# Performance work log

Measured on AMD Instinct MI355X. Metric: run time of the kernel, lower is better.

The kernel has to match this reference:

```python
import jax, jax.numpy as jnp
import numpy as np

INDEX_SHIFT = jnp.array([[0, 0], [-1, 0], [1, 0], [0, 1], [-1, 1], [1, 1], [0, -1], [-1, -1], [1, -1]], dtype=jnp.int32)
H, W = 320, 320
C = 32          # embed_dim / feat_channels (hard-coded 32 in module)
NH = 2          # head_num
HD = C // NH    # per-head dim
B, N = 4, 20000


def setup_inputs() -> dict:
    key = jax.random.key(0)
    ks = jax.random.split(key, 8)

    def coords(k):
        # unique (y, x) coords per sample so the coord->index lookup is well defined
        perm = jax.random.permutation(k, H * W)[:N]
        return jnp.stack([perm // W, perm % W], axis=-1).astype(jnp.int32)

    li_coors = jax.vmap(coords)(jax.random.split(ks[0], B))
    ra_coors = jax.vmap(coords)(jax.random.split(ks[1], B))
    li_feats = jax.random.normal(ks[2], (B, N, C), jnp.float32)
    ra_feats = jax.random.normal(ks[3], (B, N, C), jnp.float32)
    pos = jax.random.normal(ks[4], (9, C), jnp.float32) * 0.02

    s = 1.0 / np.sqrt(C)
    out = {"li_bev_feats": li_feats, "li_bev_coors": li_coors,
           "ra_bev_feats": ra_feats, "ra_bev_coors": ra_coors,
           "pos_embedding": pos}
    for i, kk in [(1, ks[5]), (2, ks[6])]:
        k0, k1 = jax.random.split(kk)
        out[f"in_w{i}"] = jax.random.uniform(k0, (3 * C, C), jnp.float32, -s, s)
        out[f"in_b{i}"] = jnp.zeros((3 * C,), jnp.float32)
        out[f"out_w{i}"] = jax.random.uniform(k1, (C, C), jnp.float32, -s, s)
        out[f"out_b{i}"] = jnp.zeros((C,), jnp.float32)
    return out


def _build_kv(q_coors, kv_coors, kv_feats, pos):
    # q_coors, kv_coors: (N,2) int; kv_feats: (N,C)
    n = q_coors.shape[0]
    grid = jnp.full((H * W,), -1, jnp.int32)
    grid = grid.at[kv_coors[:, 0] * W + kv_coors[:, 1]].set(jnp.arange(n, dtype=jnp.int32))
    sc = q_coors[None, :, :] + INDEX_SHIFT[:, None, :]            # (9,N,2)
    valid = (sc[..., 0] >= 0) & (sc[..., 0] < H) & (sc[..., 1] >= 0) & (sc[..., 1] < W)
    flat = jnp.clip(sc[..., 0], 0, H - 1) * W + jnp.clip(sc[..., 1], 0, W - 1)
    sel = jnp.where(valid, grid[flat], -1)                        # (9,N)
    mask = (sel >= 0)[..., None]                                  # (9,N,1)
    g = kv_feats[jnp.maximum(sel, 0)]                             # (9,N,C)
    k = jnp.where(mask, g, 0.0)
    v = jnp.where(mask, g + pos[:, None, :], 0.0)
    return k.transpose(1, 0, 2), v.transpose(1, 0, 2)             # (N,9,C)


def _mha(q, k, v, in_w, in_b, out_w, out_b):
    # q: (N,C); k,v: (N,L,C). torch MultiheadAttention (eval mode, dropout off).
    n, L = k.shape[0], k.shape[1]
    wq, wk, wv = in_w[:C], in_w[C:2 * C], in_w[2 * C:]
    bq, bk, bv = in_b[:C], in_b[C:2 * C], in_b[2 * C:]
    qh = (q @ wq.T + bq).reshape(n, NH, HD)
    kh = (k @ wk.T + bk).reshape(n, L, NH, HD)
    vh = (v @ wv.T + bv).reshape(n, L, NH, HD)
    scores = jnp.einsum('nhd,nlhd->nhl', qh, kh) / np.sqrt(HD)
    attn = jax.nn.softmax(scores, axis=-1)
    o = jnp.einsum('nhl,nlhd->nhd', attn, vh).reshape(n, C)
    return o @ out_w.T + out_b


def _scatter(feats, coors):
    # PointPillarsScatter: place (N,C) feats at (y,x) into a (C,H,W) canvas
    idx = coors[:, 0] * W + coors[:, 1]
    canvas = jnp.zeros((C, H * W), feats.dtype)
    return canvas.at[:, idx].set(feats.T).reshape(C, H, W)


def reference(li_bev_feats, li_bev_coors, ra_bev_feats, ra_bev_coors, pos_embedding,
              in_w1, in_b1, out_w1, out_b1, in_w2, in_b2, out_w2, out_b2):
    def one(li_f, li_c, ra_f, ra_c):
        k, v = _build_kv(li_c, ra_c, ra_f, pos_embedding)
        li_img = _scatter(_mha(li_f, k, v, in_w1, in_b1, out_w1, out_b1), li_c)
        k, v = _build_kv(ra_c, li_c, li_f, pos_embedding)
        ra_img = _scatter(_mha(ra_f, k, v, in_w2, in_b2, out_w2, out_b2), ra_c)
        return li_img, ra_img
    li_imgs, ra_imgs = jax.vmap(one)(li_bev_feats, li_bev_coors, ra_bev_feats, ra_bev_coors)
    return li_imgs, ra_imgs  # each (B, C, H, W)
```

## Files before the change

kernel.cpp:

```cpp
#include <hip/hip_runtime.h>

constexpr int Hh = 320, Ww = 320, Cc = 32, Bb = 4, Nn = 20000;
constexpr int HWp = Hh * Ww;

__global__ __launch_bounds__(256) void build_grid_k(
    const int* __restrict__ li_coors, const int* __restrict__ ra_coors,
    int* __restrict__ grids) {
  int idx = blockIdx.x * 256 + threadIdx.x;
  if (idx >= 2 * Bb * Nn) return;
  int src = idx / (Bb * Nn);
  int r = idx - src * (Bb * Nn);
  int b = r / Nn, n = r - b * Nn;
  const int* c = (src == 0 ? li_coors : ra_coors) + ((size_t)b * Nn + n) * 2;
  grids[((size_t)src * Bb + b) * HWp + c[0] * Ww + c[1]] = n;
}

__global__ __launch_bounds__(256) void posv_k(
    const float* __restrict__ pos, const float* __restrict__ in_w1,
    const float* __restrict__ in_w2, float* __restrict__ posv) {
  int t = blockIdx.x * 256 + threadIdx.x;
  if (t >= 2 * 9 * Cc) return;
  int dir = t / (9 * Cc);
  int rem = t - dir * 9 * Cc;
  int l = rem / Cc, ch = rem - l * Cc;
  const float* w = (dir == 0 ? in_w1 : in_w2) + (2 * Cc + ch) * Cc;
  const float* pl = pos + l * Cc;
  float acc = 0.f;
  for (int j = 0; j < Cc; j++) acc += pl[j] * w[j];
  posv[t] = acc;
}

__global__ __launch_bounds__(256) void project_qkv_k(
    const float* __restrict__ li_feats, const float* __restrict__ ra_feats,
    const float* __restrict__ in_w1, const float* __restrict__ in_b1,
    const float* __restrict__ in_w2, const float* __restrict__ in_b2,
    float* __restrict__ Qh, float* __restrict__ Kp, float* __restrict__ Vp) {
  int sb = blockIdx.y;
  int src = sb >> 2, b = sb & 3;
  __shared__ __align__(16) float wqT[32 * 36];
  __shared__ __align__(16) float wkT[32 * 36];
  __shared__ __align__(16) float wvT[32 * 36];
  __shared__ float bq[Cc];
  const float* wA = src == 0 ? in_w1 : in_w2;
  const float* bA = src == 0 ? in_b1 : in_b2;
  const float* wB = src == 0 ? in_w2 : in_w1;
  int t = threadIdx.x;
  for (int i = t; i < Cc * Cc; i += 256) {
    int c = i >> 5, j = i & 31;
    wqT[j * 36 + c] = wA[i];
    wkT[j * 36 + c] = wB[Cc * Cc + i];
    wvT[j * 36 + c] = wB[2 * Cc * Cc + i];
  }
  if (t < Cc) bq[t] = bA[t];
  __syncthreads();
  int pl = t >> 3, c4 = t & 7;
  int n = blockIdx.x * 32 + pl;
  const float* f = (src == 0 ? li_feats : ra_feats) + ((size_t)b * Nn + n) * Cc;
  float fv[32];
  const float4* fp = (const float4*)f;
#pragma unroll
  for (int j4 = 0; j4 < 8; j4++) {
    float4 v = fp[j4];
    fv[4 * j4 + 0] = v.x; fv[4 * j4 + 1] = v.y;
    fv[4 * j4 + 2] = v.z; fv[4 * j4 + 3] = v.w;
  }
  const float4* wq4 = (const float4*)wqT;
  const float4* wk4 = (const float4*)wkT;
  const float4* wv4 = (const float4*)wvT;
  float4 aq = *(const float4*)(bq + c4 * 4);
  float4 ak = make_float4(0.f, 0.f, 0.f, 0.f);
  float4 av = make_float4(0.f, 0.f, 0.f, 0.f);
#pragma unroll
  for (int j = 0; j < 32; j++) {
    float fj = fv[j];
    float4 q4 = wq4[j * 9 + c4];
    float4 k4 = wk4[j * 9 + c4];
    float4 v4 = wv4[j * 9 + c4];
    aq.x += fj * q4.x; aq.y += fj * q4.y; aq.z += fj * q4.z; aq.w += fj * q4.w;
    ak.x += fj * k4.x; ak.y += fj * k4.y; ak.z += fj * k4.z; ak.w += fj * k4.w;
    av.x += fj * v4.x; av.y += fj * v4.y; av.z += fj * v4.z; av.w += fj * v4.w;
  }
  int dirq = src, dirkv = 1 - src;
  size_t qbase = (((size_t)dirq * Bb + b) * Nn + n) * Cc + c4 * 4;
  size_t kvbase = (((size_t)dirkv * Bb + b) * Nn + n) * Cc + c4 * 4;
  *(float4*)(Qh + qbase) = aq;
  *(float4*)(Kp + kvbase) = ak;
  *(float4*)(Vp + kvbase) = av;
}

__global__ __launch_bounds__(256) void attn_k(
    const int* __restrict__ li_coors, const int* __restrict__ ra_coors,
    const int* __restrict__ grids, const float* __restrict__ Qh,
    const float* __restrict__ Kp, const float* __restrict__ Vp,
    const float* __restrict__ posv, const float* __restrict__ in_b1,
    const float* __restrict__ in_b2, const float* __restrict__ out_w1,
    const float* __restrict__ out_b1, const float* __restrict__ out_w2,
    const float* __restrict__ out_b2, float* __restrict__ out_pts) {
  int db = blockIdx.y;
  int dir = db >> 2, b = db & 3;
  __shared__ __align__(16) float ow[Cc * Cc];
  __shared__ __align__(16) float pv[9 * Cc];
  __shared__ float obias[Cc], bk[Cc], bv[Cc];
  const float* owp = dir == 0 ? out_w1 : out_w2;
  const float* obp = dir == 0 ? out_b1 : out_b2;
  const float* ibp = dir == 0 ? in_b1 : in_b2;
  int t = threadIdx.x;
  for (int i = t; i < Cc * Cc; i += 256) ow[i] = owp[i];
  for (int i = t; i < 9 * Cc; i += 256) pv[i] = posv[dir * 9 * Cc + i];
  if (t < Cc) { obias[t] = obp[t]; bk[t] = ibp[Cc + t]; bv[t] = ibp[2 * Cc + t]; }
  __syncthreads();
  int n = blockIdx.x * 256 + t;
  if (n >= Nn) return;
  const int* qc = (dir == 0 ? li_coors : ra_coors) + ((size_t)b * Nn + n) * 2;
  int y = qc[0], x = qc[1];
  const int* g = grids + ((size_t)(1 - dir) * Bb + b) * HWp;
  float4 qh4[8];
  const float4* qp = (const float4*)(Qh + (((size_t)dir * Bb + b) * Nn + n) * Cc);
#pragma unroll
  for (int j = 0; j < 8; j++) qh4[j] = qp[j];
  float sinv0 = 0.f, sinv1 = 0.f;
  const float4* bk4 = (const float4*)bk;
#pragma unroll
  for (int j4 = 0; j4 < 4; j4++) {
    float4 b4 = bk4[j4], q4 = qh4[j4];
    sinv0 += q4.x * b4.x + q4.y * b4.y + q4.z * b4.z + q4.w * b4.w;
  }
#pragma unroll
  for (int j4 = 4; j4 < 8; j4++) {
    float4 b4 = bk4[j4], q4 = qh4[j4];
    sinv1 += q4.x * b4.x + q4.y * b4.y + q4.z * b4.z + q4.w * b4.w;
  }
  sinv0 *= 0.25f;
  sinv1 *= 0.25f;
  const int DY[9] = {0, -1, 1, 0, -1, 1, 0, -1, 1};
  const int DX[9] = {0, 0, 0, 1, 1, 1, -1, -1, -1};
  int sel[9];
  float s0[9], s1[9];
  const float* Kpb = Kp + ((size_t)dir * Bb + b) * Nn * Cc;
#pragma unroll
  for (int l = 0; l < 9; l++) {
    int cy = y + DY[l], cx = x + DX[l];
    int se = -1;
    if ((unsigned)cy < (unsigned)Hh && (unsigned)cx < (unsigned)Ww) se = g[cy * Ww + cx];
    sel[l] = se;
    float d0 = 0.f, d1 = 0.f;
    if (se >= 0) {
      const float4* kp = (const float4*)(Kpb + (size_t)se * Cc);
#pragma unroll
      for (int j4 = 0; j4 < 4; j4++) {
        float4 k4 = kp[j4], q4 = qh4[j4];
        d0 += q4.x * k4.x + q4.y * k4.y + q4.z * k4.z + q4.w * k4.w;
      }
#pragma unroll
      for (int j4 = 4; j4 < 8; j4++) {
        float4 k4 = kp[j4], q4 = qh4[j4];
        d1 += q4.x * k4.x + q4.y * k4.y + q4.z * k4.z + q4.w * k4.w;
      }
    }
    s0[l] = sinv0 + 0.25f * d0;
    s1[l] = sinv1 + 0.25f * d1;
  }
  float m0 = s0[0], m1 = s1[0];
#pragma unroll
  for (int l = 1; l < 9; l++) { m0 = fmaxf(m0, s0[l]); m1 = fmaxf(m1, s1[l]); }
  float sum0 = 0.f, sum1 = 0.f;
#pragma unroll
  for (int l = 0; l < 9; l++) {
    s0[l] = __expf(s0[l] - m0);
    s1[l] = __expf(s1[l] - m1);
    sum0 += s0[l];
    sum1 += s1[l];
  }
  float o[Cc];
#pragma unroll
  for (int j = 0; j < Cc; j++) o[j] = 0.f;
  const float* Vpb = Vp + ((size_t)dir * Bb + b) * Nn * Cc;
  const float4* pv4 = (const float4*)pv;
#pragma unroll
  for (int l = 0; l < 9; l++) {
    int se = sel[l];
    if (se >= 0) {
      const float4* vp = (const float4*)(Vpb + (size_t)se * Cc);
      float w0 = s0[l], w1 = s1[l];
#pragma unroll
      for (int j4 = 0; j4 < 8; j4++) {
        float4 v4 = vp[j4];
        float4 p4 = pv4[l * 8 + j4];
        float w = (j4 < 4) ? w0 : w1;
        o[j4 * 4 + 0] += w * (v4.x + p4.x);
        o[j4 * 4 + 1] += w * (v4.y + p4.y);
        o[j4 * 4 + 2] += w * (v4.z + p4.z);
        o[j4 * 4 + 3] += w * (v4.w + p4.w);
      }
    }
  }
  float r0 = 1.f / sum0, r1 = 1.f / sum1;
#pragma unroll
  for (int j = 0; j < 16; j++) o[j] = o[j] * r0 + bv[j];
#pragma unroll
  for (int j = 16; j < Cc; j++) o[j] = o[j] * r1 + bv[j];
  float* op = out_pts + (((size_t)dir * Bb + b) * Nn + n) * Cc;
  const float4* ow4 = (const float4*)ow;
#pragma unroll
  for (int c0 = 0; c0 < Cc; c0 += 4) {
    float a[4];
#pragma unroll
    for (int u = 0; u < 4; u++) {
      float acc = obias[c0 + u];
#pragma unroll
      for (int j4 = 0; j4 < 8; j4++) {
        float4 w4 = ow4[(c0 + u) * 8 + j4];
        acc += o[j4 * 4 + 0] * w4.x + o[j4 * 4 + 1] * w4.y + o[j4 * 4 + 2] * w4.z +
               o[j4 * 4 + 3] * w4.w;
      }
      a[u] = acc;
    }
    *(float4*)(op + c0) = make_float4(a[0], a[1], a[2], a[3]);
  }
}

__global__ __launch_bounds__(256) void scatter_k(
    const int* __restrict__ grids, const float* __restrict__ out_pts,
    float* __restrict__ out) {
  int db = blockIdx.y;
  int dir = db >> 2, b = db & 3;
  int p = blockIdx.x * 256 + threadIdx.x;
  const int* g = grids + ((size_t)dir * Bb + b) * HWp;
  int se = g[p];
  float* ob = out + (((size_t)dir * Bb + b) * Cc) * HWp + p;
  if (se < 0) {
#pragma unroll
    for (int c = 0; c < Cc; c++) ob[(size_t)c * HWp] = 0.f;
  } else {
    const float4* sp =
        (const float4*)(out_pts + (((size_t)dir * Bb + b) * Nn + se) * Cc);
#pragma unroll
    for (int c4 = 0; c4 < 8; c4++) {
      float4 v = sp[c4];
      ob[(size_t)(c4 * 4 + 0) * HWp] = v.x;
      ob[(size_t)(c4 * 4 + 1) * HWp] = v.y;
      ob[(size_t)(c4 * 4 + 2) * HWp] = v.z;
      ob[(size_t)(c4 * 4 + 3) * HWp] = v.w;
    }
  }
}

extern "C" void kernel_launch(void* const* d_in, const int* in_sizes, int n_in,
                              void* d_out, int out_size, void* d_ws, size_t ws_size,
                              hipStream_t stream) {
  const float* li_feats = (const float*)d_in[0];
  const int* li_coors = (const int*)d_in[1];
  const float* ra_feats = (const float*)d_in[2];
  const int* ra_coors = (const int*)d_in[3];
  const float* pos = (const float*)d_in[4];
  const float* in_w1 = (const float*)d_in[5];
  const float* in_b1 = (const float*)d_in[6];
  const float* out_w1 = (const float*)d_in[7];
  const float* out_b1 = (const float*)d_in[8];
  const float* in_w2 = (const float*)d_in[9];
  const float* in_b2 = (const float*)d_in[10];
  const float* out_w2 = (const float*)d_in[11];
  const float* out_b2 = (const float*)d_in[12];

  char* ws = (char*)d_ws;
  size_t off = 0;
  int* grids = (int*)(ws + off);
  off += (size_t)2 * Bb * HWp * 4;
  float* Qh = (float*)(ws + off);
  off += (size_t)2 * Bb * Nn * Cc * 4;
  float* Kp = (float*)(ws + off);
  off += (size_t)2 * Bb * Nn * Cc * 4;
  float* Vp = (float*)(ws + off);
  off += (size_t)2 * Bb * Nn * Cc * 4;
  float* out_pts = (float*)(ws + off);
  off += (size_t)2 * Bb * Nn * Cc * 4;
  float* posv = (float*)(ws + off);
  off += (size_t)2 * 9 * Cc * 4;

  hipMemsetAsync(grids, 0xFF, (size_t)2 * Bb * HWp * 4, stream);
  build_grid_k<<<(2 * Bb * Nn + 255) / 256, 256, 0, stream>>>(li_coors, ra_coors,
                                                              grids);
  posv_k<<<3, 256, 0, stream>>>(pos, in_w1, in_w2, posv);
  dim3 gkv(Nn / 32, 2 * Bb);
  project_qkv_k<<<gkv, 256, 0, stream>>>(li_feats, ra_feats, in_w1, in_b1, in_w2,
                                         in_b2, Qh, Kp, Vp);
  dim3 ga((Nn + 255) / 256, 2 * Bb);
  attn_k<<<ga, 256, 0, stream>>>(li_coors, ra_coors, grids, Qh, Kp, Vp, posv, in_b1,
                                 in_b2, out_w1, out_b1, out_w2, out_b2, out_pts);
  dim3 gs(HWp / 256, 2 * Bb);
  scatter_k<<<gs, 256, 0, stream>>>(grids, out_pts, (float*)d_out);
}
```

Measured before the change: 105.1 us.

## Fuse all stages into one persistent kernel with grid barriers, drop grid memset

Merges grid build, positional projection, QKV projection, attention and scatter into one persistent kernel of 768 blocks separated by atomic grid-wide barriers. This removes several launches and the large memset of the index grids. Stale grid entries are instead caught by checking the stored index's coordinates against the cell. The QKV projection now computes four points per thread so weight loads from shared memory are reused. In exchange, correctness depends on all 768 blocks being co-resident, and every lookup now does an extra coordinate read.

```diff
diff --git a/kernel.cpp b/kernel.cpp
--- a/kernel.cpp
+++ b/kernel.cpp
@@ -2,245 +2,301 @@
 
 constexpr int Hh = 320, Ww = 320, Cc = 32, Bb = 4, Nn = 20000;
 constexpr int HWp = Hh * Ww;
-
-__global__ __launch_bounds__(256) void build_grid_k(
+constexpr int NB = 768;
+constexpr int PROJ_BLOCKS_PER_SB = 157;
+constexpr int PROJ_TOTAL = PROJ_BLOCKS_PER_SB * 8;
+constexpr int BUILD_BLOCKS = 625;
+constexpr int P1_TOTAL = PROJ_TOTAL + BUILD_BLOCKS + 3;
+constexpr int ATTN_PER_SB = 79;
+constexpr int P2_TOTAL = ATTN_PER_SB * 8;
+
+__device__ __forceinline__ void gbar(int* cnt, int* flg) {
+  __syncthreads();
+  if (threadIdx.x == 0) {
+    __threadfence();
+    if (atomicAdd(cnt, 1) == NB - 1) {
+      atomicExch(flg, 1);
+    } else {
+      while (atomicAdd(flg, 0) == 0) __builtin_amdgcn_s_sleep(8);
+    }
+    __threadfence();
+  }
+  __syncthreads();
+}
+
+__global__ __launch_bounds__(256, 3) void mega_k(
+    const float* __restrict__ li_feats, const float* __restrict__ ra_feats,
     const int* __restrict__ li_coors, const int* __restrict__ ra_coors,
-    int* __restrict__ grids) {
-  int idx = blockIdx.x * 256 + threadIdx.x;
-  if (idx >= 2 * Bb * Nn) return;
-  int src = idx / (Bb * Nn);
-  int r = idx - src * (Bb * Nn);
-  int b = r / Nn, n = r - b * Nn;
-  const int* c = (src == 0 ? li_coors : ra_coors) + ((size_t)b * Nn + n) * 2;
-  grids[((size_t)src * Bb + b) * HWp + c[0] * Ww + c[1]] = n;
-}
-
-__global__ __launch_bounds__(256) void posv_k(
-    const float* __restrict__ pos, const float* __restrict__ in_w1,
-    const float* __restrict__ in_w2, float* __restrict__ posv) {
-  int t = blockIdx.x * 256 + threadIdx.x;
-  if (t >= 2 * 9 * Cc) return;
-  int dir = t / (9 * Cc);
-  int rem = t - dir * 9 * Cc;
-  int l = rem / Cc, ch = rem - l * Cc;
-  const float* w = (dir == 0 ? in_w1 : in_w2) + (2 * Cc + ch) * Cc;
-  const float* pl = pos + l * Cc;
-  float acc = 0.f;
-  for (int j = 0; j < Cc; j++) acc += pl[j] * w[j];
-  posv[t] = acc;
-}
-
-__global__ __launch_bounds__(256) void project_qkv_k(
-    const float* __restrict__ li_feats, const float* __restrict__ ra_feats,
+    const float* __restrict__ pos,
     const float* __restrict__ in_w1, const float* __restrict__ in_b1,
+    const float* __restrict__ out_w1, const float* __restrict__ out_b1,
     const float* __restrict__ in_w2, const float* __restrict__ in_b2,
-    float* __restrict__ Qh, float* __restrict__ Kp, float* __restrict__ Vp) {
-  int sb = blockIdx.y;
-  int src = sb >> 2, b = sb & 3;
-  __shared__ __align__(16) float wqT[32 * 36];
-  __shared__ __align__(16) float wkT[32 * 36];
-  __shared__ __align__(16) float wvT[32 * 36];
+    const float* __restrict__ out_w2, const float* __restrict__ out_b2,
+    int* __restrict__ grids, float* __restrict__ Qh, float* __restrict__ Kp,
+    float* __restrict__ Vp, float* __restrict__ out_pts,
+    float* __restrict__ posv, int* __restrict__ bars,
+    float* __restrict__ out) {
+  __shared__ __align__(16) float wqT[32 * 36], wkT[32 * 36], wvT[32 * 36];
   __shared__ float bq[Cc];
-  const float* wA = src == 0 ? in_w1 : in_w2;
-  const float* bA = src == 0 ? in_b1 : in_b2;
-  const float* wB = src == 0 ? in_w2 : in_w1;
+  __shared__ __align__(16) float ow[Cc * Cc], pvs[9 * Cc];
+  __shared__ float obias[Cc], bk[Cc], bv[Cc];
   int t = threadIdx.x;
-  for (int i = t; i < Cc * Cc; i += 256) {
-    int c = i >> 5, j = i & 31;
-    wqT[j * 36 + c] = wA[i];
-    wkT[j * 36 + c] = wB[Cc * Cc + i];
-    wvT[j * 36 + c] = wB[2 * Cc * Cc + i];
+  int bid = blockIdx.x;
+
+  for (int vb = bid; vb < P1_TOTAL; vb += NB) {
+    if (vb < PROJ_TOTAL) {
+      int sb = vb / PROJ_BLOCKS_PER_SB;
+      int blk = vb - sb * PROJ_BLOCKS_PER_SB;
+      int src = sb >> 2, b = sb & 3;
+      const float* wA = src == 0 ? in_w1 : in_w2;
+      const float* bA = src == 0 ? in_b1 : in_b2;
+      const float* wB = src == 0 ? in_w2 : in_w1;
+      __syncthreads();
+      for (int i = t; i < Cc * Cc; i += 256) {
+        int c = i >> 5, j = i & 31;
+        wqT[j * 36 + c] = wA[i];
+        wkT[j * 36 + c] = wB[Cc * Cc + i];
+        wvT[j * 36 + c] = wB[2 * Cc * Cc + i];
+      }
+      if (t < Cc) bq[t] = bA[t];
+      __syncthreads();
+      int quad = t >> 3, c4 = t & 7;
+      int n0 = blk * 128 + quad * 4;
+      if (n0 + 4 > Nn) n0 = Nn - 4;
+      const float* f =
+          (src == 0 ? li_feats : ra_feats) + ((size_t)b * Nn + n0) * Cc;
+      const float4* wq4 = (const float4*)wqT;
+      const float4* wk4 = (const float4*)wkT;
+      const float4* wv4 = (const float4*)wvT;
+      float4 bq4 = *(const float4*)(bq + c4 * 4);
+      float4 aq[4], ak[4], av[4];
+#pragma unroll
+      for (int i = 0; i < 4; i++) {
+        aq[i] = bq4;
+        ak[i] = make_float4(0.f, 0.f, 0.f, 0.f);
+        av[i] = make_float4(0.f, 0.f, 0.f, 0.f);
+      }
+#pragma unroll
+      for (int j4 = 0; j4 < 8; j4++) {
+        float fjs[4][4];
+#pragma unroll
+        for (int i = 0; i < 4; i++) {
+          float4 v = ((const float4*)(f + i * Cc))[j4];
+          fjs[i][0] = v.x; fjs[i][1] = v.y; fjs[i][2] = v.z; fjs[i][3] = v.w;
+        }
+#pragma unroll
+        for (int u = 0; u < 4; u++) {
+          int j = j4 * 4 + u;
+          float4 q4 = wq4[j * 9 + c4];
+          float4 k4 = wk4[j * 9 + c4];
+          float4 v4 = wv4[j * 9 + c4];
+#pragma unroll
+          for (int i = 0; i < 4; i++) {
+            float fj = fjs[i][u];
+            aq[i].x += fj * q4.x; aq[i].y += fj * q4.y;
+            aq[i].z += fj * q4.z; aq[i].w += fj * q4.w;
+            ak[i].x += fj * k4.x; ak[i].y += fj * k4.y;
+            ak[i].z += fj * k4.z; ak[i].w += fj * k4.w;
+            av[i].x += fj * v4.x; av[i].y += fj * v4.y;
+            av[i].z += fj * v4.z; av[i].w += fj * v4.w;
+          }
+        }
+      }
+      int dirq = src, dirkv = 1 - src;
+      size_t qbase = (((size_t)dirq * Bb + b) * Nn + n0) * Cc + c4 * 4;
+      size_t kvbase = (((size_t)dirkv * Bb + b) * Nn + n0) * Cc + c4 * 4;
+#pragma unroll
+      for (int i = 0; i < 4; i++) {
+        *(float4*)(Qh + qbase + i * Cc) = aq[i];
+        *(float4*)(Kp + kvbase + i * Cc) = ak[i];
+        *(float4*)(Vp + kvbase + i * Cc) = av[i];
+      }
+    } else if (vb < PROJ_TOTAL + BUILD_BLOCKS) {
+      int idx = (vb - PROJ_TOTAL) * 256 + t;
+      int src = idx / (Bb * Nn);
+      int r = idx - src * (Bb * Nn);
+      int b = r / Nn, n = r - b * Nn;
+      const int* c = (src == 0 ? li_coors : ra_coors) + ((size_t)b * Nn + n) * 2;
+      grids[((size_t)src * Bb + b) * HWp + c[0] * Ww + c[1]] = n;
+    } else {
+      int tt = (vb - PROJ_TOTAL - BUILD_BLOCKS) * 256 + t;
+      if (tt < 2 * 9 * Cc) {
+        int dir = tt / (9 * Cc);
+        int rem = tt - dir * 9 * Cc;
+        int l = rem / Cc, ch = rem - l * Cc;
+        const float* w = (dir == 0 ? in_w1 : in_w2) + (2 * Cc + ch) * Cc;
+        const float* pl = pos + l * Cc;
+        float acc = 0.f;
+        for (int j = 0; j < Cc; j++) acc += pl[j] * w[j];
+        posv[tt] = acc;
+      }
+    }
   }
-  if (t < Cc) bq[t] = bA[t];
-  __syncthreads();
-  int pl = t >> 3, c4 = t & 7;
-  int n = blockIdx.x * 32 + pl;
-  const float* f = (src == 0 ? li_feats : ra_feats) + ((size_t)b * Nn + n) * Cc;
-  float fv[32];
-  const float4* fp = (const float4*)f;
-#pragma unroll
-  for (int j4 = 0; j4 < 8; j4++) {
-    float4 v = fp[j4];
-    fv[4 * j4 + 0] = v.x; fv[4 * j4 + 1] = v.y;
-    fv[4 * j4 + 2] = v.z; fv[4 * j4 + 3] = v.w;
+  gbar(&bars[0], &bars[1]);
+
+  if (bid < P2_TOTAL) {
+    int db = bid / ATTN_PER_SB;
+    int bx = bid - db * ATTN_PER_SB;
+    int dir = db >> 2, b = db & 3;
+    const float* owp = dir == 0 ? out_w1 : out_w2;
+    const float* obp = dir == 0 ? out_b1 : out_b2;
+    const float* ibp = dir == 0 ? in_b1 : in_b2;
+    for (int i = t; i < Cc * Cc; i += 256) ow[i] = owp[i];
+    for (int i = t; i < 9 * Cc; i += 256) pvs[i] = posv[dir * 9 * Cc + i];
+    if (t < Cc) {
+      obias[t] = obp[t]; bk[t] = ibp[Cc + t]; bv[t] = ibp[2 * Cc + t];
+    }
+    __syncthreads();
+    int n = bx * 256 + t;
+    if (n < Nn) {
+      const int* qc = (dir == 0 ? li_coors : ra_coors) + ((size_t)b * Nn + n) * 2;
+      int y = qc[0], x = qc[1];
+      const int* g = grids + ((size_t)(1 - dir) * Bb + b) * HWp;
+      const int2* kvc =
+          (const int2*)((dir == 0 ? ra_coors : li_coors) + (size_t)b * Nn * 2);
+      float4 qh4[8];
+      const float4* qp =
+          (const float4*)(Qh + (((size_t)dir * Bb + b) * Nn + n) * Cc);
+#pragma unroll
+      for (int j = 0; j < 8; j++) qh4[j] = qp[j];
+      float sinv0 = 0.f, sinv1 = 0.f;
+      const float4* bk4 = (const float4*)bk;
+#pragma unroll
+      for (int j4 = 0; j4 < 4; j4++) {
+        float4 b4 = bk4[j4], q4 = qh4[j4];
+        sinv0 += q4.x * b4.x + q4.y * b4.y + q4.z * b4.z + q4.w * b4.w;
+      }
+#pragma unroll
+      for (int j4 = 4; j4 < 8; j4++) {
+        float4 b4 = bk4[j4], q4 = qh4[j4];
+        sinv1 += q4.x * b4.x + q4.y * b4.y + q4.z * b4.z + q4.w * b4.w;
+      }
+      sinv0 *= 0.25f;
+      sinv1 *= 0.25f;
+      const int DY[9] = {0, -1, 1, 0, -1, 1, 0, -1, 1};
+      const int DX[9] = {0, 0, 0, 1, 1, 1, -1, -1, -1};
+      int sel[9];
+      float s0[9], s1[9];
+      const float* Kpb = Kp + ((size_t)dir * Bb + b) * Nn * Cc;
+#pragma unroll
+      for (int l = 0; l < 9; l++) {
+        int cy = y + DY[l], cx = x + DX[l];
+        int se = -1;
+        if ((unsigned)cy < (unsigned)Hh && (unsigned)cx < (unsigned)Ww) {
+          int cand = g[cy * Ww + cx];
+          if (cand >= 0 && cand < Nn) {
+            int2 cc2 = kvc[cand];
+            if (cc2.x == cy && cc2.y == cx) se = cand;
+          }
+        }
+        sel[l] = se;
+        float d0 = 0.f, d1 = 0.f;
+        if (se >= 0) {
+          const float4* kp = (const float4*)(Kpb + (size_t)se * Cc);
+#pragma unroll
+          for (int j4 = 0; j4 < 4; j4++) {
+            float4 k4 = kp[j4], q4 = qh4[j4];
+            d0 += q4.x * k4.x + q4.y * k4.y + q4.z * k4.z + q4.w * k4.w;
+          }
+#pragma unroll
+          for (int j4 = 4; j4 < 8; j4++) {
+            float4 k4 = kp[j4], q4 = qh4[j4];
+            d1 += q4.x * k4.x + q4.y * k4.y + q4.z * k4.z + q4.w * k4.w;
+          }
+        }
+        s0[l] = sinv0 + 0.25f * d0;
+        s1[l] = sinv1 + 0.25f * d1;
+      }
+      float m0 = s0[0], m1 = s1[0];
+#pragma unroll
+      for (int l = 1; l < 9; l++) { m0 = fmaxf(m0, s0[l]); m1 = fmaxf(m1, s1[l]); }
+      float sum0 = 0.f, sum1 = 0.f;
+#pragma unroll
+      for (int l = 0; l < 9; l++) {
+        s0[l] = __expf(s0[l] - m0);
+        s1[l] = __expf(s1[l] - m1);
+        sum0 += s0[l];
+        sum1 += s1[l];
+      }
+      float o[Cc];
+#pragma unroll
+      for (int j = 0; j < Cc; j++) o[j] = 0.f;
+      const float* Vpb = Vp + ((size_t)dir * Bb + b) * Nn * Cc;
+      const float4* pv4 = (const float4*)pvs;
+#pragma unroll
+      for (int l = 0; l < 9; l++) {
+        int se = sel[l];
+        if (se >= 0) {
+          const float4* vp = (const float4*)(Vpb + (size_t)se * Cc);
+          float w0 = s0[l], w1 = s1[l];
+#pragma unroll
+          for (int j4 = 0; j4 < 8; j4++) {
+            float4 v4 = vp[j4];
+            float4 p4 = pv4[l * 8 + j4];
+            float w = (j4 < 4) ? w0 : w1;
+            o[j4 * 4 + 0] += w * (v4.x + p4.x);
+            o[j4 * 4 + 1] += w * (v4.y + p4.y);
+            o[j4 * 4 + 2] += w * (v4.z + p4.z);
+            o[j4 * 4 + 3] += w * (v4.w + p4.w);
+          }
+        }
+      }
+      float r0 = 1.f / sum0, r1 = 1.f / sum1;
+#pragma unroll
+      for (int j = 0; j < 16; j++) o[j] = o[j] * r0 + bv[j];
+#pragma unroll
+      for (int j = 16; j < Cc; j++) o[j] = o[j] * r1 + bv[j];
+      float* op = out_pts + (((size_t)dir * Bb + b) * Nn + n) * Cc;
+      const float4* ow4 = (const float4*)ow;
+#pragma unroll
+      for (int c0 = 0; c0 < Cc; c0 += 4) {
+        float a[4];
+#pragma unroll
+        for (int u = 0; u < 4; u++) {
+          float acc = obias[c0 + u];
+#pragma unroll
+          for (int j4 = 0; j4 < 8; j4++) {
+            float4 w4 = ow4[(c0 + u) * 8 + j4];
+            acc += o[j4 * 4 + 0] * w4.x + o[j4 * 4 + 1] * w4.y +
+                   o[j4 * 4 + 2] * w4.z + o[j4 * 4 + 3] * w4.w;
+          }
+          a[u] = acc;
+        }
+        *(float4*)(op + c0) = make_float4(a[0], a[1], a[2], a[3]);
+      }
+    }
   }
-  const float4* wq4 = (const float4*)wqT;
-  const float4* wk4 = (const float4*)wkT;
-  const float4* wv4 = (const float4*)wvT;
-  float4 aq = *(const float4*)(bq + c4 * 4);
-  float4 ak = make_float4(0.f, 0.f, 0.f, 0.f);
-  float4 av = make_float4(0.f, 0.f, 0.f, 0.f);
-#pragma unroll
-  for (int j = 0; j < 32; j++) {
-    float fj = fv[j];
-    float4 q4 = wq4[j * 9 + c4];
-    float4 k4 = wk4[j * 9 + c4];
-    float4 v4 = wv4[j * 9 + c4];
-    aq.x += fj * q4.x; aq.y += fj * q4.y; aq.z += fj * q4.z; aq.w += fj * q4.w;
-    ak.x += fj * k4.x; ak.y += fj * k4.y; ak.z += fj * k4.z; ak.w += fj * k4.w;
-    av.x += fj * v4.x; av.y += fj * v4.y; av.z += fj * v4.z; av.w += fj * v4.w;
-  }
-  int dirq = src, dirkv = 1 - src;
-  size_t qbase = (((size_t)dirq * Bb + b) * Nn + n) * Cc + c4 * 4;
-  size_t kvbase = (((size_t)dirkv * Bb + b) * Nn + n) * Cc + c4 * 4;
-  *(float4*)(Qh + qbase) = aq;
-  *(float4*)(Kp + kvbase) = ak;
-  *(float4*)(Vp + kvbase) = av;
-}
-
-__global__ __launch_bounds__(256) void attn_k(
-    const int* __restrict__ li_coors, const int* __restrict__ ra_coors,
-    const int* __restrict__ grids, const float* __restrict__ Qh,
-    const float* __restrict__ Kp, const float* __restrict__ Vp,
-    const float* __restrict__ posv, const float* __restrict__ in_b1,
-    const float* __restrict__ in_b2, const float* __restrict__ out_w1,
-    const float* __restrict__ out_b1, const float* __restrict__ out_w2,
-    const float* __restrict__ out_b2, float* __restrict__ out_pts) {
-  int db = blockIdx.y;
-  int dir = db >> 2, b = db & 3;
-  __shared__ __align__(16) float ow[Cc * Cc];
-  __shared__ __align__(16) float pv[9 * Cc];
-  __shared__ float obias[Cc], bk[Cc], bv[Cc];
-  const float* owp = dir == 0 ? out_w1 : out_w2;
-  const float* obp = dir == 0 ? out_b1 : out_b2;
-  const float* ibp = dir == 0 ? in_b1 : in_b2;
-  int t = threadIdx.x;
-  for (int i = t; i < Cc * Cc; i += 256) ow[i] = owp[i];
-  for (int i = t; i < 9 * Cc; i += 256) pv[i] = posv[dir * 9 * Cc + i];
-  if (t < Cc) { obias[t] = obp[t]; bk[t] = ibp[Cc + t]; bv[t] = ibp[2 * Cc + t]; }
-  __syncthreads();
-  int n = blockIdx.x * 256 + t;
-  if (n >= Nn) return;
-  const int* qc = (dir == 0 ? li_coors : ra_coors) + ((size_t)b * Nn + n) * 2;
-  int y = qc[0], x = qc[1];
-  const int* g = grids + ((size_t)(1 - dir) * Bb + b) * HWp;
-  float4 qh4[8];
-  const float4* qp = (const float4*)(Qh + (((size_t)dir * Bb + b) * Nn + n) * Cc);
-#pragma unroll
-  for (int j = 0; j < 8; j++) qh4[j] = qp[j];
-  float sinv0 = 0.f, sinv1 = 0.f;
-  const float4* bk4 = (const float4*)bk;
-#pragma unroll
-  for (int j4 = 0; j4 < 4; j4++) {
-    float4 b4 = bk4[j4], q4 = qh4[j4];
-    sinv0 += q4.x * b4.x + q4.y * b4.y + q4.z * b4.z + q4.w * b4.w;
-  }
-#pragma unroll
-  for (int j4 = 4; j4 < 8; j4++) {
-    float4 b4 = bk4[j4], q4 = qh4[j4];
-    sinv1 += q4.x * b4.x + q4.y * b4.y + q4.z * b4.z + q4.w * b4.w;
-  }
-  sinv0 *= 0.25f;
-  sinv1 *= 0.25f;
-  const int DY[9] = {0, -1, 1, 0, -1, 1, 0, -1, 1};
-  const int DX[9] = {0, 0, 0, 1, 1, 1, -1, -1, -1};
-  int sel[9];
-  float s0[9], s1[9];
-  const float* Kpb = Kp + ((size_t)dir * Bb + b) * Nn * Cc;
-#pragma unroll
-  for (int l = 0; l < 9; l++) {
-    int cy = y + DY[l], cx = x + DX[l];
-    int se = -1;
-    if ((unsigned)cy < (unsigned)Hh && (unsigned)cx < (unsigned)Ww) se = g[cy * Ww + cx];
-    sel[l] = se;
-    float d0 = 0.f, d1 = 0.f;
-    if (se >= 0) {
-      const float4* kp = (const float4*)(Kpb + (size_t)se * Cc);
-#pragma unroll
-      for (int j4 = 0; j4 < 4; j4++) {
-        float4 k4 = kp[j4], q4 = qh4[j4];
-        d0 += q4.x * k4.x + q4.y * k4.y + q4.z * k4.z + q4.w * k4.w;
-      }
-#pragma unroll
-      for (int j4 = 4; j4 < 8; j4++) {
-        float4 k4 = kp[j4], q4 = qh4[j4];
-        d1 += q4.x * k4.x + q4.y * k4.y + q4.z * k4.z + q4.w * k4.w;
-      }
-    }
-    s0[l] = sinv0 + 0.25f * d0;
-    s1[l] = sinv1 + 0.25f * d1;
-  }
-  float m0 = s0[0], m1 = s1[0];
-#pragma unroll
-  for (int l = 1; l < 9; l++) { m0 = fmaxf(m0, s0[l]); m1 = fmaxf(m1, s1[l]); }
-  float sum0 = 0.f, sum1 = 0.f;
-#pragma unroll
-  for (int l = 0; l < 9; l++) {
-    s0[l] = __expf(s0[l] - m0);
-    s1[l] = __expf(s1[l] - m1);
-    sum0 += s0[l];
-    sum1 += s1[l];
-  }
-  float o[Cc];
-#pragma unroll
-  for (int j = 0; j < Cc; j++) o[j] = 0.f;
-  const float* Vpb = Vp + ((size_t)dir * Bb + b) * Nn * Cc;
-  const float4* pv4 = (const float4*)pv;
-#pragma unroll
-  for (int l = 0; l < 9; l++) {
-    int se = sel[l];
-    if (se >= 0) {
-      const float4* vp = (const float4*)(Vpb + (size_t)se * Cc);
-      float w0 = s0[l], w1 = s1[l];
-#pragma unroll
-      for (int j4 = 0; j4 < 8; j4++) {
-        float4 v4 = vp[j4];
-        float4 p4 = pv4[l * 8 + j4];
-        float w = (j4 < 4) ? w0 : w1;
-        o[j4 * 4 + 0] += w * (v4.x + p4.x);
-        o[j4 * 4 + 1] += w * (v4.y + p4.y);
-        o[j4 * 4 + 2] += w * (v4.z + p4.z);
-        o[j4 * 4 + 3] += w * (v4.w + p4.w);
-      }
-    }
-  }
-  float r0 = 1.f / sum0, r1 = 1.f / sum1;
-#pragma unroll
-  for (int j = 0; j < 16; j++) o[j] = o[j] * r0 + bv[j];
-#pragma unroll
-  for (int j = 16; j < Cc; j++) o[j] = o[j] * r1 + bv[j];
-  float* op = out_pts + (((size_t)dir * Bb + b) * Nn + n) * Cc;
-  const float4* ow4 = (const float4*)ow;
-#pragma unroll
-  for (int c0 = 0; c0 < Cc; c0 += 4) {
-    float a[4];
-#pragma unroll
-    for (int u = 0; u < 4; u++) {
-      float acc = obias[c0 + u];
-#pragma unroll
-      for (int j4 = 0; j4 < 8; j4++) {
-        float4 w4 = ow4[(c0 + u) * 8 + j4];
-        acc += o[j4 * 4 + 0] * w4.x + o[j4 * 4 + 1] * w4.y + o[j4 * 4 + 2] * w4.z +
-               o[j4 * 4 + 3] * w4.w;
-      }
-      a[u] = acc;
-    }
-    *(float4*)(op + c0) = make_float4(a[0], a[1], a[2], a[3]);
-  }
-}
-
-__global__ __launch_bounds__(256) void scatter_k(
-    const int* __restrict__ grids, const float* __restrict__ out_pts,
-    float* __restrict__ out) {
-  int db = blockIdx.y;
-  int dir = db >> 2, b = db & 3;
-  int p = blockIdx.x * 256 + threadIdx.x;
-  const int* g = grids + ((size_t)dir * Bb + b) * HWp;
-  int se = g[p];
-  float* ob = out + (((size_t)dir * Bb + b) * Cc) * HWp + p;
-  if (se < 0) {
-#pragma unroll
-    for (int c = 0; c < Cc; c++) ob[(size_t)c * HWp] = 0.f;
-  } else {
-    const float4* sp =
-        (const float4*)(out_pts + (((size_t)dir * Bb + b) * Nn + se) * Cc);
-#pragma unroll
-    for (int c4 = 0; c4 < 8; c4++) {
-      float4 v = sp[c4];
-      ob[(size_t)(c4 * 4 + 0) * HWp] = v.x;
-      ob[(size_t)(c4 * 4 + 1) * HWp] = v.y;
-      ob[(size_t)(c4 * 4 + 2) * HWp] = v.z;
-      ob[(size_t)(c4 * 4 + 3) * HWp] = v.w;
+  gbar(&bars[2], &bars[3]);
+
+  int gtid = bid * 256 + t;
+  for (int i = gtid; i < 2 * Bb * HWp; i += NB * 256) {
+    int db = i / HWp;
+    int p = i - db * HWp;
+    int dir = db >> 2, b = db & 3;
+    const int* gq = grids + ((size_t)dir * Bb + b) * HWp;
+    const int2* qc2 =
+        (const int2*)((dir == 0 ? li_coors : ra_coors) + (size_t)b * Nn * 2);
+    int se = gq[p];
+    bool ok = (se >= 0 && se < Nn);
+    if (ok) {
+      int2 c2 = qc2[se];
+      ok = (c2.x * Ww + c2.y) == p;
+    }
+    float* ob = out + (((size_t)dir * Bb + b) * Cc) * HWp + p;
+    if (!ok) {
+#pragma unroll
+      for (int c = 0; c < Cc; c++) ob[(size_t)c * HWp] = 0.f;
+    } else {
+      const float4* sp =
+          (const float4*)(out_pts + (((size_t)dir * Bb + b) * Nn + se) * Cc);
+#pragma unroll
+      for (int c4 = 0; c4 < 8; c4++) {
+        float4 v = sp[c4];
+        ob[(size_t)(c4 * 4 + 0) * HWp] = v.x;
+        ob[(size_t)(c4 * 4 + 1) * HWp] = v.y;
+        ob[(size_t)(c4 * 4 + 2) * HWp] = v.z;
+        ob[(size_t)(c4 * 4 + 3) * HWp] = v.w;
+      }
     }
   }
 }
@@ -276,17 +332,12 @@
   off += (size_t)2 * Bb * Nn * Cc * 4;
   float* posv = (float*)(ws + off);
   off += (size_t)2 * 9 * Cc * 4;
-
-  hipMemsetAsync(grids, 0xFF, (size_t)2 * Bb * HWp * 4, stream);
-  build_grid_k<<<(2 * Bb * Nn + 255) / 256, 256, 0, stream>>>(li_coors, ra_coors,
-                                                              grids);
-  posv_k<<<3, 256, 0, stream>>>(pos, in_w1, in_w2, posv);
-  dim3 gkv(Nn / 32, 2 * Bb);
-  project_qkv_k<<<gkv, 256, 0, stream>>>(li_feats, ra_feats, in_w1, in_b1, in_w2,
-                                         in_b2, Qh, Kp, Vp);
-  dim3 ga((Nn + 255) / 256, 2 * Bb);
-  attn_k<<<ga, 256, 0, stream>>>(li_coors, ra_coors, grids, Qh, Kp, Vp, posv, in_b1,
-                                 in_b2, out_w1, out_b1, out_w2, out_b2, out_pts);
-  dim3 gs(HWp / 256, 2 * Bb);
-  scatter_k<<<gs, 256, 0, stream>>>(grids, out_pts, (float*)d_out);
+  int* bars = (int*)(ws + off);
+  off += 16;
+
+  hipMemsetAsync(bars, 0, 16, stream);
+  mega_k<<<NB, 256, 0, stream>>>(li_feats, ra_feats, li_coors, ra_coors, pos,
+                                 in_w1, in_b1, out_w1, out_b1, in_w2, in_b2,
+                                 out_w2, out_b2, grids, Qh, Kp, Vp, out_pts,
+                                 posv, bars, (float*)d_out);
 }
```

Result: slower. 317.2 us (+201.8%).
